# Optimization experiments

Measured on AMD Instinct MI355X. Metric: run time of the kernel, lower is better.

The kernel has to match this reference:

```python
import jax, jax.numpy as jnp
import numpy as np

DIM_PROBLEM = 256
DIM_CONTEXT = 1024
DIM_HIDDEN = 4096
INIT = 0.01


def setup_inputs() -> dict:
    key = jax.random.key(0)
    ks = jax.random.split(key, 12)
    H, C = DIM_HIDDEN, DIM_CONTEXT
    inp = {
        "context": jax.random.normal(ks[0], (C,), dtype=jnp.float32),
        "u": jax.random.uniform(ks[1], (DIM_PROBLEM,), dtype=jnp.float32),
        "l1_w": jax.random.normal(ks[2], (1, C), dtype=jnp.float32) * INIT,
        "l1_b": jnp.zeros((1,), dtype=jnp.float32),
        "Wf_w": jax.random.normal(ks[3], (H, H + 1), dtype=jnp.float32) * INIT,
        "Wf_b": jnp.zeros((H,), dtype=jnp.float32),
        "Wi_w": jax.random.normal(ks[4], (H, H + 1), dtype=jnp.float32) * INIT,
        "Wi_b": jnp.zeros((H,), dtype=jnp.float32),
        "Wc_w": jax.random.normal(ks[5], (H, H + 1), dtype=jnp.float32) * INIT,
        "Wc_b": jnp.zeros((H,), dtype=jnp.float32),
        "Wo_w": jax.random.normal(ks[6], (1, H + 1), dtype=jnp.float32) * INIT,
        "Wo_b": jnp.zeros((1,), dtype=jnp.float32),
    }
    return inp


def reference(context, u, l1_w, l1_b, Wf_w, Wf_b, Wi_w, Wi_b, Wc_w, Wc_b, Wo_w, Wo_b):
    H = Wf_w.shape[0]
    x0 = l1_w @ context + l1_b                      # (1,)
    h0 = jnp.zeros((H,), dtype=context.dtype)       # T.Tensor(H) treated as zeros
    c0 = jnp.zeros((H,), dtype=context.dtype)
    logp0 = jnp.zeros((1,), dtype=context.dtype)

    def step(carry, u_t):
        h, c, x, logp = carry
        z = jnp.concatenate([h, x])                 # (H+1,)
        f = jax.nn.sigmoid(Wf_w @ z + Wf_b)         # (H,)
        i = jax.nn.sigmoid(Wi_w @ z + Wi_b)
        cc = jnp.tanh(Wc_w @ z + Wc_b)
        o = jax.nn.sigmoid(Wo_w @ z + Wo_b)         # (1,)
        c_new = f * c + i * cc
        h_new = o * jnp.tanh(c_new)                 # broadcast (1,)*(H,)
        # detached Bernoulli(o) sample via pre-drawn uniform noise
        s = (u_t < jax.lax.stop_gradient(o)).astype(x.dtype)  # (1,)
        # log p accumulated: log(p * o^s * (1-o)^(1-s)) = logp + s*log o + (1-s)*log(1-o)
        logp_new = logp + s * jnp.log(o) + (1.0 - s) * jnp.log(1.0 - o)
        return (h_new, c_new, s, logp_new), s

    (_, _, _, logp), sol = jax.lax.scan(step, (h0, c0, x0, logp0), u)
    solution = sol[:, None, :]                      # (dim_problem, 1, 1)
    return solution, logp
```

## Files before the change

kernel.cpp:

```cpp
#include <hip/hip_runtime.h>
#include <hip/hip_fp16.h>
#include <stdint.h>


#define HID    4096
#define CTX    1024
#define NSTEPS 256
#define NBLK   256
#define TPB    1024
#define WAVES  16
#define HROWS  16
#define GROWS  48
#define RPW    3
#define NCH    8

typedef _Float16 h2 __attribute__((ext_vector_type(2)));

__device__ __forceinline__ float fdot2f(uint32_t a, uint32_t b, float c) {
#if __has_builtin(__builtin_amdgcn_fdot2)
  return __builtin_amdgcn_fdot2(__builtin_bit_cast(h2, a),
                                __builtin_bit_cast(h2, b), c, false);
#else
  h2 x = __builtin_bit_cast(h2, a), y = __builtin_bit_cast(h2, b);
  return c + (float)x[0]*(float)y[0] + (float)x[1]*(float)y[1];
#endif
}
__device__ __forceinline__ uint32_t pkf16(float x, float y) {
  h2 v; v[0] = (_Float16)x; v[1] = (_Float16)y;
  return __builtin_bit_cast(uint32_t, v);
}
__device__ __forceinline__ uint4 cvt8(const float* p) {
  return make_uint4(pkf16(p[0],p[1]), pkf16(p[2],p[3]),
                    pkf16(p[4],p[5]), pkf16(p[6],p[7]));
}
__device__ __forceinline__ float dot4(float acc, uint4 a, uint4 b) {
  acc = fdot2f(a.x, b.x, acc); acc = fdot2f(a.y, b.y, acc);
  acc = fdot2f(a.z, b.z, acc); acc = fdot2f(a.w, b.w, acc);
  return acc;
}
__device__ __forceinline__ void agw(uint32_t &slot, uint32_t v) {
  asm volatile("v_accvgpr_write_b32 %0, %1" : "=a"(slot) : "v"(v));
}
__device__ __forceinline__ uint32_t agr(uint32_t slot) {
  uint32_t v;
  asm("v_accvgpr_read_b32 %0, %1" : "=v"(v) : "a"(slot));
  return v;
}
__device__ __forceinline__ void stT(uint64_t* p, uint32_t payload, uint32_t tag) {
  const uint64_t v = ((uint64_t)tag << 32) | (uint64_t)payload;
  __hip_atomic_store(p, v, __ATOMIC_RELAXED, __HIP_MEMORY_SCOPE_AGENT);
}
__device__ __forceinline__ uint64_t ldT(const uint64_t* p) {
  return __hip_atomic_load(p, __ATOMIC_RELAXED, __HIP_MEMORY_SCOPE_AGENT);
}
__device__ __forceinline__ uint32_t waitT(const uint64_t* p, uint32_t tag) {
  uint64_t v = ldT(p);
  while ((uint32_t)(v >> 32) != tag) {
    __builtin_amdgcn_s_sleep(1);
    v = ldT(p);
  }
  return (uint32_t)v;
}

__global__ __launch_bounds__(TPB)
void lstm(const float* __restrict__ ctx, const float* __restrict__ u,
          const float* __restrict__ l1w, const float* __restrict__ l1b,
          const float* __restrict__ Wf,  const float* __restrict__ Wfb,
          const float* __restrict__ Wi,  const float* __restrict__ Wib,
          const float* __restrict__ Wc,  const float* __restrict__ Wcb,
          const float* __restrict__ Wow, const float* __restrict__ Wob,
          uint64_t* __restrict__ hh0, uint64_t* __restrict__ hh1,
          uint64_t* __restrict__ part0, uint64_t* __restrict__ part1,
          float* __restrict__ out)
{
  __shared__ uint4 wlds[WAVES][HID/8];
  __shared__ uint4 zsh4[HID/8];
  __shared__ float red[WAVES];
  __shared__ float pre[GROWS];
  __shared__ float cst[HROWS];
  __shared__ float bias[GROWS];
  __shared__ float wx[GROWS];
  __shared__ float x0sh, osh, ssh;

  const int tid  = threadIdx.x;
  const int b    = blockIdx.x;
  const int wv   = tid >> 6;
  const int lane = tid & 63;

  uint32_t* z32 = (uint32_t*)zsh4;
  for (int i = tid; i < HID/2; i += TPB) z32[i] = 0u;
  if (tid < HROWS) cst[tid] = 0.f;
  if (tid < GROWS) {
    int g = tid / HROWS, j = tid % HROWS;
    const float* bw = (g==0 ? Wfb : (g==1 ? Wib : Wcb));
    const float* gw = (g==0 ? Wf  : (g==1 ? Wi  : Wc ));
    bias[tid] = bw[b*HROWS + j];
    wx[tid]   = gw[(size_t)(b*HROWS + j)*4097 + 4096];
  }

  const float wolocal = (tid < HROWS) ? Wow[b*HROWS + tid] : 0.f;
  const float woxw = Wow[HID];
  const float wob0 = Wob[0];

  uint32_t wreg[64];
  {
    const int fl0 = wv*RPW;
    const int g0 = (fl0+0)/HROWS, j0 = (fl0+0)%HROWS;
    const int g1 = (fl0+1)/HROWS, j1 = (fl0+1)%HROWS;
    const int g2 = (fl0+2)/HROWS, j2 = (fl0+2)%HROWS;
    const float* r0 = (g0==0?Wf:(g0==1?Wi:Wc)) + (size_t)(b*HROWS+j0)*4097;
    const float* r1 = (g1==0?Wf:(g1==1?Wi:Wc)) + (size_t)(b*HROWS+j1)*4097;
    const float* r2 = (g2==0?Wf:(g2==1?Wi:Wc)) + (size_t)(b*HROWS+j2)*4097;
    #pragma unroll
    for (int c = 0; c < NCH; ++c) {
      const int col = c*512 + lane*8;
      const uint4 va = cvt8(r0 + col);
      agw(wreg[c*8+0], va.x); agw(wreg[c*8+1], va.y);
      agw(wreg[c*8+2], va.z); agw(wreg[c*8+3], va.w);
      const uint4 vb = cvt8(r1 + col);
      agw(wreg[c*8+4], vb.x); agw(wreg[c*8+5], vb.y);
      agw(wreg[c*8+6], vb.z); agw(wreg[c*8+7], vb.w);
      wlds[wv][c*64 + lane] = cvt8(r2 + col);
    }
  }

  {
    float p = l1w[tid] * ctx[tid];
    #pragma unroll
    for (int off = 32; off; off >>= 1) p += __shfl_down(p, off, 64);
    __syncthreads();
    if (lane == 0) red[wv] = p;
    __syncthreads();
    if (tid == 0) {
      float ssum = 0.f;
      for (int w = 0; w < WAVES; ++w) ssum += red[w];
      x0sh = ssum + l1b[0];
    }
    __syncthreads();
  }
  float xcur = x0sh;
  float logp = 0.f;
  float ut = u[0];

  for (int t = 0; t < NSTEPS; ++t) {
    if (wv == 0) {
      float ps = 0.f;
      if (t > 0) {
        const uint64_t* pr = (t & 1) ? part0 : part1;
        const uint32_t tg = (uint32_t)t;
        const float q0 = __uint_as_float(waitT(&pr[lane*4+0], tg));
        const float q1 = __uint_as_float(waitT(&pr[lane*4+1], tg));
        const float q2 = __uint_as_float(waitT(&pr[lane*4+2], tg));
        const float q3 = __uint_as_float(waitT(&pr[lane*4+3], tg));
        ps = ((q0 + q1) + q2) + q3;
      }
      #pragma unroll
      for (int off = 32; off; off >>= 1) ps += __shfl_down(ps, off, 64);
      if (lane == 0) {
        const float opre = ps + woxw*xcur + wob0;
        const float o = 1.f / (1.f + expf(-opre));
        osh = o;
        ssh = (ut < o) ? 1.f : 0.f;
      }
    }

    float a0 = 0.f, a1 = 0.f, a2 = 0.f;
    #pragma unroll
    for (int c = 0; c < NCH; ++c) {
      const uint4 zz = zsh4[c*64 + lane];
      const uint4 wl = wlds[wv][c*64 + lane];
      a0 = fdot2f(agr(wreg[c*8+0]), zz.x, a0);
      a0 = fdot2f(agr(wreg[c*8+1]), zz.y, a0);
      a0 = fdot2f(agr(wreg[c*8+2]), zz.z, a0);
      a0 = fdot2f(agr(wreg[c*8+3]), zz.w, a0);
      a1 = fdot2f(agr(wreg[c*8+4]), zz.x, a1);
      a1 = fdot2f(agr(wreg[c*8+5]), zz.y, a1);
      a1 = fdot2f(agr(wreg[c*8+6]), zz.z, a1);
      a1 = fdot2f(agr(wreg[c*8+7]), zz.w, a1);
      a2 = dot4(a2, wl, zz);
    }
    #pragma unroll
    for (int off = 32; off; off >>= 1) {
      a0 += __shfl_down(a0, off, 64);
      a1 += __shfl_down(a1, off, 64);
      a2 += __shfl_down(a2, off, 64);
    }
    if (lane == 0) {
      const int fl = wv*RPW;
      pre[fl+0] = a0 + wx[fl+0]*xcur + bias[fl+0];
      pre[fl+1] = a1 + wx[fl+1]*xcur + bias[fl+1];
      pre[fl+2] = a2 + wx[fl+2]*xcur + bias[fl+2];
    }
    __syncthreads();

    const float o = osh;
    const float s = ssh;
    uint64_t* hwH = (t & 1) ? hh1 : hh0;
    uint64_t* pwF = (t & 1) ? part1 : part0;
    float hv = 0.f;
    if (tid < HROWS) {
      const float ff = 1.f / (1.f + expf(-pre[tid]));
      const float ii = 1.f / (1.f + expf(-pre[HROWS+tid]));
      const float cc = tanhf(pre[2*HROWS+tid]);
      const float cn = ff*cst[tid] + ii*cc;
      cst[tid] = cn;
      hv = o * tanhf(cn);
    }
    if (tid < 64) {
      float pp = wolocal * hv;
      #pragma unroll
      for (int off = 8; off; off >>= 1) pp += __shfl_down(pp, off, 64);
      const float he = __shfl(hv, 2*(tid&7),   64);
      const float ho = __shfl(hv, 2*(tid&7)+1, 64);
      if (tid < 8) stT(&hwH[b*8 + tid], pkf16(he, ho), (uint32_t)(t+1));
      if (tid == 0) stT(&pwF[b], __float_as_uint(pp), (uint32_t)(t+1));
    }
    if (b == 0 && tid == 0) {
      logp += (s != 0.f) ? logf(o) : logf(1.f - o);
      out[t] = s;
    }
    xcur = s;

    if (t + 1 < NSTEPS) {
      const uint64_t* hr2 = (t & 1) ? hh1 : hh0;
      const uint32_t tg = (uint32_t)(t+1);
      uint64_t v0 = ldT(&hr2[tid]);
      uint64_t v1 = ldT(&hr2[tid + TPB]);
      while ((uint32_t)(v0 >> 32) != tg) {
        __builtin_amdgcn_s_sleep(1); v0 = ldT(&hr2[tid]);
      }
      while ((uint32_t)(v1 >> 32) != tg) {
        __builtin_amdgcn_s_sleep(1); v1 = ldT(&hr2[tid + TPB]);
      }
      z32[tid]       = (uint32_t)v0;
      z32[tid + TPB] = (uint32_t)v1;
      ut = u[t+1];
      __syncthreads();
    }
  }
  if (b == 0 && tid == 0) out[NSTEPS] = logp;
}

extern "C" void kernel_launch(void* const* d_in, const int* in_sizes, int n_in,
                              void* d_out, int out_size, void* d_ws, size_t ws_size,
                              hipStream_t stream) {
  const float* ctx = (const float*)d_in[0];
  const float* u   = (const float*)d_in[1];
  const float* l1w = (const float*)d_in[2];
  const float* l1b = (const float*)d_in[3];
  const float* Wf  = (const float*)d_in[4];
  const float* Wfb = (const float*)d_in[5];
  const float* Wi  = (const float*)d_in[6];
  const float* Wib = (const float*)d_in[7];
  const float* Wc  = (const float*)d_in[8];
  const float* Wcb = (const float*)d_in[9];
  const float* Wow = (const float*)d_in[10];
  const float* Wob = (const float*)d_in[11];
  float* out = (float*)d_out;

  char* ws = (char*)d_ws;
  uint64_t* part0 = (uint64_t*)(ws + 4096);
  uint64_t* part1 = (uint64_t*)(ws + 8192);
  uint64_t* hh0   = (uint64_t*)(ws + 12288);
  uint64_t* hh1   = (uint64_t*)(ws + 12288 + 16384);
  (void)hipMemsetAsync(ws + 4096, 0, 40960, stream);

  lstm<<<NBLK, TPB, 0, stream>>>(ctx,u,l1w,l1b,Wf,Wfb,Wi,Wib,Wc,Wcb,Wow,Wob,
                                 hh0,hh1,part0,part1,out);
}
```

Baseline: 1.008 ms.

## Halve block size, keep all gate weights in AGPRs, replace barrier with flag sync

Blocks shrink to 512 threads with 8 waves, and each wave now holds all six gate rows (two hidden units × three gates) in 192 accumulator registers. This removes the LDS-resident weight row and the shared pre-activation array. The mid-step __syncthreads is replaced by tagged LDS flags for the output gate and per-wave partial sums, and the z vector is double-buffered, leaving one barrier per step. The partial-sum loads are issued before the dot products to hide latency. The risks are heavy AGPR pressure, since occupancy must fit 192 weight registers, and spinning on LDS flags.

```diff
diff --git a/kernel.cpp b/kernel.cpp
--- a/kernel.cpp
+++ b/kernel.cpp
@@ -7,11 +7,9 @@
 #define CTX    1024
 #define NSTEPS 256
 #define NBLK   256
-#define TPB    1024
-#define WAVES  16
+#define TPB    512
+#define WAVES  8
 #define HROWS  16
-#define GROWS  48
-#define RPW    3
 #define NCH    8
 
 typedef _Float16 h2 __attribute__((ext_vector_type(2)));
@@ -33,11 +31,6 @@
   return make_uint4(pkf16(p[0],p[1]), pkf16(p[2],p[3]),
                     pkf16(p[4],p[5]), pkf16(p[6],p[7]));
 }
-__device__ __forceinline__ float dot4(float acc, uint4 a, uint4 b) {
-  acc = fdot2f(a.x, b.x, acc); acc = fdot2f(a.y, b.y, acc);
-  acc = fdot2f(a.z, b.z, acc); acc = fdot2f(a.w, b.w, acc);
-  return acc;
-}
 __device__ __forceinline__ void agw(uint32_t &slot, uint32_t v) {
   asm volatile("v_accvgpr_write_b32 %0, %1" : "=a"(slot) : "v"(v));
 }
@@ -53,16 +46,18 @@
 __device__ __forceinline__ uint64_t ldT(const uint64_t* p) {
   return __hip_atomic_load(p, __ATOMIC_RELAXED, __HIP_MEMORY_SCOPE_AGENT);
 }
-__device__ __forceinline__ uint32_t waitT(const uint64_t* p, uint32_t tag) {
-  uint64_t v = ldT(p);
-  while ((uint32_t)(v >> 32) != tag) {
-    __builtin_amdgcn_s_sleep(1);
-    v = ldT(p);
-  }
-  return (uint32_t)v;
-}
-
-__global__ __launch_bounds__(TPB)
+__device__ __forceinline__ void stL(uint64_t* p, uint64_t v) {
+  __hip_atomic_store(p, v, __ATOMIC_RELAXED, __HIP_MEMORY_SCOPE_WORKGROUP);
+}
+__device__ __forceinline__ uint64_t ldL(const uint64_t* p) {
+  return __hip_atomic_load(p, __ATOMIC_RELAXED, __HIP_MEMORY_SCOPE_WORKGROUP);
+}
+__device__ __forceinline__ float rfl(float x) {
+  return __builtin_bit_cast(float,
+      __builtin_amdgcn_readfirstlane(__builtin_bit_cast(int, x)));
+}
+
+__global__ __launch_bounds__(TPB, 2)
 void lstm(const float* __restrict__ ctx, const float* __restrict__ u,
           const float* __restrict__ l1w, const float* __restrict__ l1b,
           const float* __restrict__ Wf,  const float* __restrict__ Wfb,
@@ -73,167 +68,183 @@
           uint64_t* __restrict__ part0, uint64_t* __restrict__ part1,
           float* __restrict__ out)
 {
-  __shared__ uint4 wlds[WAVES][HID/8];
-  __shared__ uint4 zsh4[HID/8];
-  __shared__ float red[WAVES];
-  __shared__ float pre[GROWS];
-  __shared__ float cst[HROWS];
-  __shared__ float bias[GROWS];
-  __shared__ float wx[GROWS];
-  __shared__ float x0sh, osh, ssh;
+  __shared__ uint4   zsh[2][HID/8];
+  __shared__ float    red[WAVES];
+  __shared__ float    x0sh;
+  __shared__ uint64_t osh;
+  __shared__ uint64_t pp[WAVES];
 
   const int tid  = threadIdx.x;
   const int b    = blockIdx.x;
   const int wv   = tid >> 6;
   const int lane = tid & 63;
 
-  uint32_t* z32 = (uint32_t*)zsh4;
-  for (int i = tid; i < HID/2; i += TPB) z32[i] = 0u;
-  if (tid < HROWS) cst[tid] = 0.f;
-  if (tid < GROWS) {
-    int g = tid / HROWS, j = tid % HROWS;
-    const float* bw = (g==0 ? Wfb : (g==1 ? Wib : Wcb));
-    const float* gw = (g==0 ? Wf  : (g==1 ? Wi  : Wc ));
-    bias[tid] = bw[b*HROWS + j];
-    wx[tid]   = gw[(size_t)(b*HROWS + j)*4097 + 4096];
-  }
-
-  const float wolocal = (tid < HROWS) ? Wow[b*HROWS + tid] : 0.f;
-  const float woxw = Wow[HID];
-  const float wob0 = Wob[0];
-
-  uint32_t wreg[64];
   {
-    const int fl0 = wv*RPW;
-    const int g0 = (fl0+0)/HROWS, j0 = (fl0+0)%HROWS;
-    const int g1 = (fl0+1)/HROWS, j1 = (fl0+1)%HROWS;
-    const int g2 = (fl0+2)/HROWS, j2 = (fl0+2)%HROWS;
-    const float* r0 = (g0==0?Wf:(g0==1?Wi:Wc)) + (size_t)(b*HROWS+j0)*4097;
-    const float* r1 = (g1==0?Wf:(g1==1?Wi:Wc)) + (size_t)(b*HROWS+j1)*4097;
-    const float* r2 = (g2==0?Wf:(g2==1?Wi:Wc)) + (size_t)(b*HROWS+j2)*4097;
+    uint32_t* z0 = (uint32_t*)&zsh[0][0];
+    for (int i = tid; i < HID/2; i += TPB) z0[i] = 0u;
+    if (tid == 0) osh = 0ull;
+    if (tid < WAVES) pp[tid] = 0ull;
+  }
+
+  const int hr0 = b*HROWS + 2*wv;
+  const float* rp[6] = {
+    Wf + (size_t)(hr0  )*4097, Wf + (size_t)(hr0+1)*4097,
+    Wi + (size_t)(hr0  )*4097, Wi + (size_t)(hr0+1)*4097,
+    Wc + (size_t)(hr0  )*4097, Wc + (size_t)(hr0+1)*4097 };
+
+  const float bf0 = rfl(Wfb[hr0]), bf1 = rfl(Wfb[hr0+1]);
+  const float bi0 = rfl(Wib[hr0]), bi1 = rfl(Wib[hr0+1]);
+  const float bc0 = rfl(Wcb[hr0]), bc1 = rfl(Wcb[hr0+1]);
+  const float xf0 = rfl(rp[0][HID]), xf1 = rfl(rp[1][HID]);
+  const float xi0 = rfl(rp[2][HID]), xi1 = rfl(rp[3][HID]);
+  const float xc0 = rfl(rp[4][HID]), xc1 = rfl(rp[5][HID]);
+  const float wo0 = rfl(Wow[hr0]),  wo1 = rfl(Wow[hr0+1]);
+  const float woxw = Wow[HID], wobv = Wob[0];
+
+  uint32_t wreg[192];
+  #pragma unroll
+  for (int r = 0; r < 6; ++r) {
     #pragma unroll
     for (int c = 0; c < NCH; ++c) {
-      const int col = c*512 + lane*8;
-      const uint4 va = cvt8(r0 + col);
-      agw(wreg[c*8+0], va.x); agw(wreg[c*8+1], va.y);
-      agw(wreg[c*8+2], va.z); agw(wreg[c*8+3], va.w);
-      const uint4 vb = cvt8(r1 + col);
-      agw(wreg[c*8+4], vb.x); agw(wreg[c*8+5], vb.y);
-      agw(wreg[c*8+6], vb.z); agw(wreg[c*8+7], vb.w);
-      wlds[wv][c*64 + lane] = cvt8(r2 + col);
+      const uint4 v = cvt8(rp[r] + c*512 + lane*8);
+      agw(wreg[r*32+c*4+0], v.x);
+      agw(wreg[r*32+c*4+1], v.y);
+      agw(wreg[r*32+c*4+2], v.z);
+      agw(wreg[r*32+c*4+3], v.w);
     }
   }
 
   {
-    float p = l1w[tid] * ctx[tid];
+    float p = l1w[tid]*ctx[tid] + l1w[tid+TPB]*ctx[tid+TPB];
     #pragma unroll
     for (int off = 32; off; off >>= 1) p += __shfl_down(p, off, 64);
     __syncthreads();
     if (lane == 0) red[wv] = p;
     __syncthreads();
     if (tid == 0) {
-      float ssum = 0.f;
-      for (int w = 0; w < WAVES; ++w) ssum += red[w];
-      x0sh = ssum + l1b[0];
+      float s2 = 0.f;
+      for (int w = 0; w < WAVES; ++w) s2 += red[w];
+      x0sh = s2 + l1b[0];
     }
     __syncthreads();
   }
   float xcur = x0sh;
   float logp = 0.f;
   float ut = u[0];
+  float cs0 = 0.f, cs1 = 0.f;
 
   for (int t = 0; t < NSTEPS; ++t) {
+    const uint64_t* prd = (t & 1) ? part0 : part1;
+    uint64_t pv0 = 0, pv1 = 0, pv2 = 0, pv3 = 0;
+    if (wv == 0 && t > 0) {
+      pv0 = ldT(&prd[lane*4+0]); pv1 = ldT(&prd[lane*4+1]);
+      pv2 = ldT(&prd[lane*4+2]); pv3 = ldT(&prd[lane*4+3]);
+    }
+
+    float a[6] = {0.f,0.f,0.f,0.f,0.f,0.f};
+    const uint4* zb = zsh[t & 1];
+    #pragma unroll
+    for (int c = 0; c < NCH; ++c) {
+      const uint4 zz = zb[c*64 + lane];
+      const uint32_t za[4] = {zz.x, zz.y, zz.z, zz.w};
+      #pragma unroll
+      for (int r = 0; r < 6; ++r) {
+        #pragma unroll
+        for (int e = 0; e < 4; ++e)
+          a[r] = fdot2f(agr(wreg[r*32+c*4+e]), za[e], a[r]);
+      }
+    }
+    #pragma unroll
+    for (int off = 32; off; off >>= 1) {
+      #pragma unroll
+      for (int r = 0; r < 6; ++r) a[r] += __shfl_down(a[r], off, 64);
+    }
+
     if (wv == 0) {
       float ps = 0.f;
       if (t > 0) {
-        const uint64_t* pr = (t & 1) ? part0 : part1;
         const uint32_t tg = (uint32_t)t;
-        const float q0 = __uint_as_float(waitT(&pr[lane*4+0], tg));
-        const float q1 = __uint_as_float(waitT(&pr[lane*4+1], tg));
-        const float q2 = __uint_as_float(waitT(&pr[lane*4+2], tg));
-        const float q3 = __uint_as_float(waitT(&pr[lane*4+3], tg));
+        while ((uint32_t)(pv0 >> 32) != tg) { __builtin_amdgcn_s_sleep(1); pv0 = ldT(&prd[lane*4+0]); }
+        while ((uint32_t)(pv1 >> 32) != tg) { __builtin_amdgcn_s_sleep(1); pv1 = ldT(&prd[lane*4+1]); }
+        while ((uint32_t)(pv2 >> 32) != tg) { __builtin_amdgcn_s_sleep(1); pv2 = ldT(&prd[lane*4+2]); }
+        while ((uint32_t)(pv3 >> 32) != tg) { __builtin_amdgcn_s_sleep(1); pv3 = ldT(&prd[lane*4+3]); }
+        const float q0 = __uint_as_float((uint32_t)pv0);
+        const float q1 = __uint_as_float((uint32_t)pv1);
+        const float q2 = __uint_as_float((uint32_t)pv2);
+        const float q3 = __uint_as_float((uint32_t)pv3);
         ps = ((q0 + q1) + q2) + q3;
       }
       #pragma unroll
       for (int off = 32; off; off >>= 1) ps += __shfl_down(ps, off, 64);
       if (lane == 0) {
-        const float opre = ps + woxw*xcur + wob0;
+        const float opre = ps + woxw*xcur + wobv;
         const float o = 1.f / (1.f + expf(-opre));
-        osh = o;
-        ssh = (ut < o) ? 1.f : 0.f;
-      }
-    }
-
-    float a0 = 0.f, a1 = 0.f, a2 = 0.f;
-    #pragma unroll
-    for (int c = 0; c < NCH; ++c) {
-      const uint4 zz = zsh4[c*64 + lane];
-      const uint4 wl = wlds[wv][c*64 + lane];
-      a0 = fdot2f(agr(wreg[c*8+0]), zz.x, a0);
-      a0 = fdot2f(agr(wreg[c*8+1]), zz.y, a0);
-      a0 = fdot2f(agr(wreg[c*8+2]), zz.z, a0);
-      a0 = fdot2f(agr(wreg[c*8+3]), zz.w, a0);
-      a1 = fdot2f(agr(wreg[c*8+4]), zz.x, a1);
-      a1 = fdot2f(agr(wreg[c*8+5]), zz.y, a1);
-      a1 = fdot2f(agr(wreg[c*8+6]), zz.z, a1);
-      a1 = fdot2f(agr(wreg[c*8+7]), zz.w, a1);
-      a2 = dot4(a2, wl, zz);
-    }
-    #pragma unroll
-    for (int off = 32; off; off >>= 1) {
-      a0 += __shfl_down(a0, off, 64);
-      a1 += __shfl_down(a1, off, 64);
-      a2 += __shfl_down(a2, off, 64);
-    }
+        stL(&osh, ((uint64_t)(uint32_t)(t+1) << 32) | (uint64_t)__float_as_uint(o));
+      }
+    }
+
+    uint64_t* hw = (t & 1) ? hh1 : hh0;
+    uint64_t* pw = (t & 1) ? part1 : part0;
     if (lane == 0) {
-      const int fl = wv*RPW;
-      pre[fl+0] = a0 + wx[fl+0]*xcur + bias[fl+0];
-      pre[fl+1] = a1 + wx[fl+1]*xcur + bias[fl+1];
-      pre[fl+2] = a2 + wx[fl+2]*xcur + bias[fl+2];
-    }
-    __syncthreads();
-
-    const float o = osh;
-    const float s = ssh;
-    uint64_t* hwH = (t & 1) ? hh1 : hh0;
-    uint64_t* pwF = (t & 1) ? part1 : part0;
-    float hv = 0.f;
-    if (tid < HROWS) {
-      const float ff = 1.f / (1.f + expf(-pre[tid]));
-      const float ii = 1.f / (1.f + expf(-pre[HROWS+tid]));
-      const float cc = tanhf(pre[2*HROWS+tid]);
-      const float cn = ff*cst[tid] + ii*cc;
-      cst[tid] = cn;
-      hv = o * tanhf(cn);
-    }
-    if (tid < 64) {
-      float pp = wolocal * hv;
-      #pragma unroll
-      for (int off = 8; off; off >>= 1) pp += __shfl_down(pp, off, 64);
-      const float he = __shfl(hv, 2*(tid&7),   64);
-      const float ho = __shfl(hv, 2*(tid&7)+1, 64);
-      if (tid < 8) stT(&hwH[b*8 + tid], pkf16(he, ho), (uint32_t)(t+1));
-      if (tid == 0) stT(&pwF[b], __float_as_uint(pp), (uint32_t)(t+1));
-    }
-    if (b == 0 && tid == 0) {
-      logp += (s != 0.f) ? logf(o) : logf(1.f - o);
-      out[t] = s;
-    }
-    xcur = s;
+      uint64_t ov = ldL(&osh);
+      while ((uint32_t)(ov >> 32) != (uint32_t)(t+1)) {
+        __builtin_amdgcn_s_sleep(1); ov = ldL(&osh);
+      }
+      const float o = __uint_as_float((uint32_t)ov);
+      const float s = (ut < o) ? 1.f : 0.f;
+      const float pf0 = a[0] + xf0*xcur + bf0;
+      const float pf1 = a[1] + xf1*xcur + bf1;
+      const float pi0 = a[2] + xi0*xcur + bi0;
+      const float pi1 = a[3] + xi1*xcur + bi1;
+      const float pc0 = a[4] + xc0*xcur + bc0;
+      const float pc1 = a[5] + xc1*xcur + bc1;
+      const float ff0 = 1.f/(1.f+expf(-pf0)), ff1 = 1.f/(1.f+expf(-pf1));
+      const float ii0 = 1.f/(1.f+expf(-pi0)), ii1 = 1.f/(1.f+expf(-pi1));
+      const float cc0 = tanhf(pc0), cc1 = tanhf(pc1);
+      cs0 = ff0*cs0 + ii0*cc0;
+      cs1 = ff1*cs1 + ii1*cc1;
+      const float hv0 = o*tanhf(cs0), hv1 = o*tanhf(cs1);
+      stT(&hw[b*8 + wv], pkf16(hv0, hv1), (uint32_t)(t+1));
+      const float ppv = wo0*hv0 + wo1*hv1;
+      stL(&pp[wv], ((uint64_t)(uint32_t)(t+1) << 32) | (uint64_t)__float_as_uint(ppv));
+      xcur = s;
+      if (b == 0 && wv == 0) {
+        logp += (s != 0.f) ? logf(o) : logf(1.f - o);
+        out[t] = s;
+      }
+    }
+
+    if (wv == 0) {
+      float v = 0.f;
+      if (lane < WAVES) {
+        uint64_t e = ldL(&pp[lane]);
+        while ((uint32_t)(e >> 32) != (uint32_t)(t+1)) {
+          __builtin_amdgcn_s_sleep(1); e = ldL(&pp[lane]);
+        }
+        v = __uint_as_float((uint32_t)e);
+      }
+      v += __shfl_down(v, 4, 64);
+      v += __shfl_down(v, 2, 64);
+      v += __shfl_down(v, 1, 64);
+      if (lane == 0) stT(&pw[b], __float_as_uint(v), (uint32_t)(t+1));
+    }
 
     if (t + 1 < NSTEPS) {
-      const uint64_t* hr2 = (t & 1) ? hh1 : hh0;
+      const uint64_t* hr = (t & 1) ? hh1 : hh0;
       const uint32_t tg = (uint32_t)(t+1);
-      uint64_t v0 = ldT(&hr2[tid]);
-      uint64_t v1 = ldT(&hr2[tid + TPB]);
-      while ((uint32_t)(v0 >> 32) != tg) {
-        __builtin_amdgcn_s_sleep(1); v0 = ldT(&hr2[tid]);
-      }
-      while ((uint32_t)(v1 >> 32) != tg) {
-        __builtin_amdgcn_s_sleep(1); v1 = ldT(&hr2[tid + TPB]);
-      }
-      z32[tid]       = (uint32_t)v0;
-      z32[tid + TPB] = (uint32_t)v1;
+      uint64_t v0 = ldT(&hr[tid]);
+      uint64_t v1 = ldT(&hr[tid +   TPB]);
+      uint64_t v2 = ldT(&hr[tid + 2*TPB]);
+      uint64_t v3 = ldT(&hr[tid + 3*TPB]);
+      while ((uint32_t)(v0 >> 32) != tg) { __builtin_amdgcn_s_sleep(1); v0 = ldT(&hr[tid]); }
+      while ((uint32_t)(v1 >> 32) != tg) { __builtin_amdgcn_s_sleep(1); v1 = ldT(&hr[tid +   TPB]); }
+      while ((uint32_t)(v2 >> 32) != tg) { __builtin_amdgcn_s_sleep(1); v2 = ldT(&hr[tid + 2*TPB]); }
+      while ((uint32_t)(v3 >> 32) != tg) { __builtin_amdgcn_s_sleep(1); v3 = ldT(&hr[tid + 3*TPB]); }
+      uint32_t* zn = (uint32_t*)&zsh[(t+1) & 1][0];
+      zn[tid]         = (uint32_t)v0;
+      zn[tid +   TPB] = (uint32_t)v1;
+      zn[tid + 2*TPB] = (uint32_t)v2;
+      zn[tid + 3*TPB] = (uint32_t)v3;
       ut = u[t+1];
       __syncthreads();
     }
```

Measured after the change: 1.680 ms. 66.7% more time.
